# Kernel tuning notes

Measured on AMD Instinct MI355X. Metric: run time of the kernel, lower is better.

Reference implementation:

```python
import jax, jax.numpy as jnp
import numpy as np

EMBED = 768
HEADS = 32
HEAD_DIM = EMBED // HEADS  # 24
T = 512
B = 16


def setup_inputs() -> dict:
    key = jax.random.key(0)
    ks = jax.random.split(key, 10)
    s = 1.0 / np.sqrt(EMBED)
    inp = {
        "query": jax.random.normal(ks[0], (T, B, EMBED), dtype=jnp.float32),
        "attn_bias": jax.random.normal(ks[1], (B * HEADS, T, T), dtype=jnp.float32),
        "Wq": jax.random.normal(ks[2], (EMBED, EMBED), dtype=jnp.float32) * s,
        "bq": jnp.zeros((EMBED,), dtype=jnp.float32),
        "Wk": jax.random.normal(ks[3], (EMBED, EMBED), dtype=jnp.float32) * s,
        "bk": jnp.zeros((EMBED,), dtype=jnp.float32),
        "Wv": jax.random.normal(ks[4], (EMBED, EMBED), dtype=jnp.float32) * s,
        "bv": jnp.zeros((EMBED,), dtype=jnp.float32),
        "Wo": jax.random.normal(ks[5], (EMBED, EMBED), dtype=jnp.float32) * s,
        "bo": jnp.zeros((EMBED,), dtype=jnp.float32),
    }
    return inp


def _split_heads(x):
    # [T, B, E] -> [B, H, T, d]
    t, b, _ = x.shape
    return x.reshape(t, b, HEADS, HEAD_DIM).transpose(1, 2, 0, 3)


def reference(query, attn_bias, Wq, bq, Wk, bk, Wv, bv, Wo, bo):
    t, b, e = query.shape
    scaling = HEAD_DIM ** (-0.5)
    # projections (torch Linear: x @ W.T + b)
    q = (query @ Wq.T + bq) * scaling
    k = query @ Wk.T + bk
    v = query @ Wv.T + bv
    qh, kh, vh = _split_heads(q), _split_heads(k), _split_heads(v)  # [B,H,T,d]
    scores = jnp.einsum('bhtd,bhsd->bhts', qh, kh)
    scores = scores + attn_bias.reshape(b, HEADS, t, t)
    probs = jax.nn.softmax(scores, axis=-1)  # dropout = identity (eval)
    attn = jnp.einsum('bhts,bhsd->bhtd', probs, vh)  # [B,H,T,d]
    attn = attn.transpose(2, 0, 1, 3).reshape(t, b, e)  # [T,B,E]
    out = attn @ Wo.T + bo  # final dropout = identity (eval)
    return out
```

## Files before the change

### kernel.cpp

```cpp
#include <hip/hip_runtime.h>
#include <hip/hip_bf16.h>

#define T_SEQ 512
#define BATCH 16
#define EMB 768
#define HEADS 32
#define HDIM 24
#define ROWS (T_SEQ * BATCH)
#define SCALING 0.20412414523193154f

__global__ __launch_bounds__(256)
void qkv_proj_kernel(const float* __restrict__ X,
                     const float* __restrict__ Wq, const float* __restrict__ Wk,
                     const float* __restrict__ Wv,
                     const float* __restrict__ bq, const float* __restrict__ bk,
                     const float* __restrict__ bv,
                     float* __restrict__ qo, float* __restrict__ ko,
                     float* __restrict__ vo)
{
    __shared__ float Xs[64][17];
    __shared__ __attribute__((aligned(16))) float Ws[16][68];

    const int tid = threadIdx.x;
    const int r0 = blockIdx.x * 64;
    const int nb = blockIdx.y;
    const int which = nb / 12;
    const int n0 = (nb % 12) * 64;
    const float* W    = (which == 0) ? Wq : (which == 1) ? Wk : Wv;
    const float* bias = (which == 0) ? bq : (which == 1) ? bk : bv;
    float* out        = (which == 0) ? qo : (which == 1) ? ko : vo;

    const int lrow = tid >> 2;
    const int lcol = (tid & 3) << 2;
    const int tx = tid & 15;
    const int ty = tid >> 4;

    float acc[4][4] = {};

    for (int k0 = 0; k0 < EMB; k0 += 16) {
        const float4 xv = *(const float4*)(X + (size_t)(r0 + lrow) * EMB + k0 + lcol);
        const float4 wv = *(const float4*)(W + (size_t)(n0 + lrow) * EMB + k0 + lcol);
        Xs[lrow][lcol + 0] = xv.x; Xs[lrow][lcol + 1] = xv.y;
        Xs[lrow][lcol + 2] = xv.z; Xs[lrow][lcol + 3] = xv.w;
        Ws[lcol + 0][lrow] = wv.x; Ws[lcol + 1][lrow] = wv.y;
        Ws[lcol + 2][lrow] = wv.z; Ws[lcol + 3][lrow] = wv.w;
        __syncthreads();
#pragma unroll
        for (int kk = 0; kk < 16; ++kk) {
            const float4 b4 = *(const float4*)&Ws[kk][tx * 4];
            const float a0 = Xs[ty * 4 + 0][kk];
            const float a1 = Xs[ty * 4 + 1][kk];
            const float a2 = Xs[ty * 4 + 2][kk];
            const float a3 = Xs[ty * 4 + 3][kk];
            acc[0][0] += a0 * b4.x; acc[0][1] += a0 * b4.y; acc[0][2] += a0 * b4.z; acc[0][3] += a0 * b4.w;
            acc[1][0] += a1 * b4.x; acc[1][1] += a1 * b4.y; acc[1][2] += a1 * b4.z; acc[1][3] += a1 * b4.w;
            acc[2][0] += a2 * b4.x; acc[2][1] += a2 * b4.y; acc[2][2] += a2 * b4.z; acc[2][3] += a2 * b4.w;
            acc[3][0] += a3 * b4.x; acc[3][1] += a3 * b4.y; acc[3][2] += a3 * b4.z; acc[3][3] += a3 * b4.w;
        }
        __syncthreads();
    }

#pragma unroll
    for (int ii = 0; ii < 4; ++ii) {
        const int rr = r0 + ty * 4 + ii;
        const int t = rr >> 4;
        const int b = rr & 15;
#pragma unroll
        for (int jj = 0; jj < 4; ++jj) {
            const int nn = n0 + tx * 4 + jj;
            float c = acc[ii][jj] + bias[nn];
            if (which == 0) c *= SCALING;
            const int h = nn / HDIM;
            const int dd = nn - h * HDIM;
            out[((size_t)((b * HEADS + h) * T_SEQ + t)) * HDIM + dd] = c;
        }
    }
}

__global__ __launch_bounds__(256)
void attn_kernel(const float* __restrict__ qb, const float* __restrict__ kb,
                 const float* __restrict__ vb, const float* __restrict__ bias,
                 float* __restrict__ attn)
{
    const int bh = blockIdx.x;
    const int t0 = blockIdx.y * 16;
    const int tid = threadIdx.x;

    __shared__ float Qs[16][25];
    __shared__ float Ss[16][513];
    __shared__ float red[16][17];
    __shared__ float rowm[16];
    __shared__ float rowl[16];

    const float* Kb = kb + (size_t)bh * T_SEQ * HDIM;
    const float* Vb = vb + (size_t)bh * T_SEQ * HDIM;
    const float* Bb = bias + (size_t)bh * T_SEQ * T_SEQ + (size_t)t0 * T_SEQ;

    for (int e = tid; e < 16 * HDIM; e += 256) {
        const int i = e / HDIM, dd = e - i * HDIM;
        Qs[i][dd] = qb[((size_t)bh * T_SEQ + t0 + i) * HDIM + dd];
    }
    __syncthreads();

    for (int e = tid; e < 16 * T_SEQ; e += 256) {
        const int i = e >> 9, s = e & 511;
        const float* kr = Kb + s * HDIM;
        float d = 0.f;
#pragma unroll
        for (int dd = 0; dd < HDIM; ++dd) d += Qs[i][dd] * kr[dd];
        Ss[i][s] = d + Bb[i * T_SEQ + s];
    }
    __syncthreads();

    const int i = tid >> 4;
    const int g = tid & 15;
    float m = -1e30f;
    for (int s = g; s < T_SEQ; s += 16) m = fmaxf(m, Ss[i][s]);
    red[i][g] = m;
    __syncthreads();
    if (g == 0) {
        float mm = red[i][0];
#pragma unroll
        for (int j = 1; j < 16; ++j) mm = fmaxf(mm, red[i][j]);
        rowm[i] = mm;
    }
    __syncthreads();
    const float mrow = rowm[i];
    float l = 0.f;
    for (int s = g; s < T_SEQ; s += 16) {
        const float p = __expf(Ss[i][s] - mrow);
        Ss[i][s] = p;
        l += p;
    }
    red[i][g] = l;
    __syncthreads();
    if (g == 0) {
        float ll = 0.f;
#pragma unroll
        for (int j = 0; j < 16; ++j) ll += red[i][j];
        rowl[i] = 1.f / ll;
    }
    __syncthreads();

    for (int p = tid; p < 16 * HDIM; p += 256) {
        const int ii = p / HDIM, dd = p - ii * HDIM;
        float accv = 0.f;
        const float* vp = Vb + dd;
#pragma unroll 8
        for (int s = 0; s < T_SEQ; ++s) accv += Ss[ii][s] * vp[s * HDIM];
        accv *= rowl[ii];
        const int t = t0 + ii;
        const int b = bh >> 5;
        const int h = bh & 31;
        attn[((size_t)(t * BATCH + b)) * EMB + h * HDIM + dd] = accv;
    }
}

__global__ __launch_bounds__(256)
void out_proj_kernel(const float* __restrict__ A, const float* __restrict__ Wo,
                     const float* __restrict__ bo, float* __restrict__ out)
{
    __shared__ float Xs[64][17];
    __shared__ __attribute__((aligned(16))) float Ws[16][68];

    const int tid = threadIdx.x;
    const int r0 = blockIdx.x * 64;
    const int n0 = blockIdx.y * 64;

    const int lrow = tid >> 2;
    const int lcol = (tid & 3) << 2;
    const int tx = tid & 15;
    const int ty = tid >> 4;

    float acc[4][4] = {};

    for (int k0 = 0; k0 < EMB; k0 += 16) {
        const float4 xv = *(const float4*)(A + (size_t)(r0 + lrow) * EMB + k0 + lcol);
        const float4 wv = *(const float4*)(Wo + (size_t)(n0 + lrow) * EMB + k0 + lcol);
        Xs[lrow][lcol + 0] = xv.x; Xs[lrow][lcol + 1] = xv.y;
        Xs[lrow][lcol + 2] = xv.z; Xs[lrow][lcol + 3] = xv.w;
        Ws[lcol + 0][lrow] = wv.x; Ws[lcol + 1][lrow] = wv.y;
        Ws[lcol + 2][lrow] = wv.z; Ws[lcol + 3][lrow] = wv.w;
        __syncthreads();
#pragma unroll
        for (int kk = 0; kk < 16; ++kk) {
            const float4 b4 = *(const float4*)&Ws[kk][tx * 4];
            const float a0 = Xs[ty * 4 + 0][kk];
            const float a1 = Xs[ty * 4 + 1][kk];
            const float a2 = Xs[ty * 4 + 2][kk];
            const float a3 = Xs[ty * 4 + 3][kk];
            acc[0][0] += a0 * b4.x; acc[0][1] += a0 * b4.y; acc[0][2] += a0 * b4.z; acc[0][3] += a0 * b4.w;
            acc[1][0] += a1 * b4.x; acc[1][1] += a1 * b4.y; acc[1][2] += a1 * b4.z; acc[1][3] += a1 * b4.w;
            acc[2][0] += a2 * b4.x; acc[2][1] += a2 * b4.y; acc[2][2] += a2 * b4.z; acc[2][3] += a2 * b4.w;
            acc[3][0] += a3 * b4.x; acc[3][1] += a3 * b4.y; acc[3][2] += a3 * b4.z; acc[3][3] += a3 * b4.w;
        }
        __syncthreads();
    }

#pragma unroll
    for (int ii = 0; ii < 4; ++ii) {
        const int rr = r0 + ty * 4 + ii;
#pragma unroll
        for (int jj = 0; jj < 4; ++jj) {
            const int nn = n0 + tx * 4 + jj;
            out[(size_t)rr * EMB + nn] = acc[ii][jj] + bo[nn];
        }
    }
}

extern "C" void kernel_launch(void* const* d_in, const int* in_sizes, int n_in,
                              void* d_out, int out_size, void* d_ws, size_t ws_size,
                              hipStream_t stream)
{
    const float* query = (const float*)d_in[0];
    const float* abias = (const float*)d_in[1];
    const float* Wq = (const float*)d_in[2];
    const float* bq = (const float*)d_in[3];
    const float* Wk = (const float*)d_in[4];
    const float* bk = (const float*)d_in[5];
    const float* Wv = (const float*)d_in[6];
    const float* bv = (const float*)d_in[7];
    const float* Wo = (const float*)d_in[8];
    const float* bo = (const float*)d_in[9];
    float* out = (float*)d_out;

    float* ws = (float*)d_ws;
    const size_t QKV_ELEMS = (size_t)BATCH * HEADS * T_SEQ * HDIM;
    float* qb = ws;
    float* kb = ws + QKV_ELEMS;
    float* vb = ws + 2 * QKV_ELEMS;
    float* ab = ws + 3 * QKV_ELEMS;

    dim3 gA(ROWS / 64, 36);
    qkv_proj_kernel<<<gA, 256, 0, stream>>>(query, Wq, Wk, Wv, bq, bk, bv, qb, kb, vb);

    dim3 gB(BATCH * HEADS, T_SEQ / 16);
    attn_kernel<<<gB, 256, 0, stream>>>(qb, kb, vb, abias, ab);

    dim3 gC(ROWS / 64, EMB / 64);
    out_proj_kernel<<<gC, 256, 0, stream>>>(ab, Wo, bo, out);
}
```

Measured before the change: 2.357 ms.

## Stage K and V tiles in shared memory and restructure attention thread mapping

The attention kernel now loads K and V in 128-row tiles into shared memory with vectorized float4 loads, instead of having every thread read K and V rows straight from global memory. Each QK thread computes four scores per float4 bias load, and the block grows to 384 threads so each thread owns one (row, dim) output for PV. The grid is reordered so consecutive blocks share the same head, which should improve L2 reuse of K and V. The cost is extra shared memory and barriers, plus idle threads during the softmax phase.

```diff
diff --git a/kernel.cpp b/kernel.cpp
--- a/kernel.cpp
+++ b/kernel.cpp
@@ -77,17 +77,18 @@
     }
 }
 
-__global__ __launch_bounds__(256)
+__global__ __launch_bounds__(384)
 void attn_kernel(const float* __restrict__ qb, const float* __restrict__ kb,
                  const float* __restrict__ vb, const float* __restrict__ bias,
                  float* __restrict__ attn)
 {
-    const int bh = blockIdx.x;
-    const int t0 = blockIdx.y * 16;
+    const int t0 = blockIdx.x * 16;
+    const int bh = blockIdx.y;
     const int tid = threadIdx.x;
 
     __shared__ float Qs[16][25];
-    __shared__ float Ss[16][513];
+    __shared__ float Ss[16][521];
+    __shared__ __attribute__((aligned(16))) float Ts[128][28];
     __shared__ float red[16][17];
     __shared__ float rowm[16];
     __shared__ float rowl[16];
@@ -96,64 +97,101 @@
     const float* Vb = vb + (size_t)bh * T_SEQ * HDIM;
     const float* Bb = bias + (size_t)bh * T_SEQ * T_SEQ + (size_t)t0 * T_SEQ;
 
-    for (int e = tid; e < 16 * HDIM; e += 256) {
-        const int i = e / HDIM, dd = e - i * HDIM;
+    {
+        const int i = tid / HDIM, dd = tid - i * HDIM;
         Qs[i][dd] = qb[((size_t)bh * T_SEQ + t0 + i) * HDIM + dd];
     }
     __syncthreads();
 
-    for (int e = tid; e < 16 * T_SEQ; e += 256) {
-        const int i = e >> 9, s = e & 511;
-        const float* kr = Kb + s * HDIM;
-        float d = 0.f;
-#pragma unroll
-        for (int dd = 0; dd < HDIM; ++dd) d += Qs[i][dd] * kr[dd];
-        Ss[i][s] = d + Bb[i * T_SEQ + s];
-    }
-    __syncthreads();
-
-    const int i = tid >> 4;
-    const int g = tid & 15;
-    float m = -1e30f;
-    for (int s = g; s < T_SEQ; s += 16) m = fmaxf(m, Ss[i][s]);
-    red[i][g] = m;
-    __syncthreads();
-    if (g == 0) {
+    for (int tile = 0; tile < 4; ++tile) {
+        for (int fv = tid; fv < 768; fv += 384) {
+            const float4 kv = *(const float4*)(Kb + (size_t)tile * 3072 + (size_t)fv * 4);
+            const int row = fv / 6;
+            const int col = (fv - row * 6) * 4;
+            *(float4*)&Ts[row][col] = kv;
+        }
+        __syncthreads();
+        for (int f = tid; f < 512; f += 384) {
+            const int i = f >> 5;
+            const int sl = (f & 31) * 4;
+            const float4 bv = *(const float4*)(Bb + (size_t)i * T_SEQ + tile * 128 + sl);
+            float d0 = 0.f, d1 = 0.f, d2 = 0.f, d3 = 0.f;
+#pragma unroll
+            for (int dd = 0; dd < HDIM; ++dd) {
+                const float q = Qs[i][dd];
+                d0 += q * Ts[sl + 0][dd];
+                d1 += q * Ts[sl + 1][dd];
+                d2 += q * Ts[sl + 2][dd];
+                d3 += q * Ts[sl + 3][dd];
+            }
+            const int sg = tile * 128 + sl;
+            Ss[i][sg + 0] = d0 + bv.x;
+            Ss[i][sg + 1] = d1 + bv.y;
+            Ss[i][sg + 2] = d2 + bv.z;
+            Ss[i][sg + 3] = d3 + bv.w;
+        }
+        __syncthreads();
+    }
+
+    if (tid < 256) {
+        const int i = tid >> 4;
+        const int g = tid & 15;
+        float m = -1e30f;
+        for (int s = g; s < T_SEQ; s += 16) m = fmaxf(m, Ss[i][s]);
+        red[i][g] = m;
+    }
+    __syncthreads();
+    if (tid < 256 && (tid & 15) == 0) {
+        const int i = tid >> 4;
         float mm = red[i][0];
 #pragma unroll
         for (int j = 1; j < 16; ++j) mm = fmaxf(mm, red[i][j]);
         rowm[i] = mm;
     }
     __syncthreads();
-    const float mrow = rowm[i];
-    float l = 0.f;
-    for (int s = g; s < T_SEQ; s += 16) {
-        const float p = __expf(Ss[i][s] - mrow);
-        Ss[i][s] = p;
-        l += p;
-    }
-    red[i][g] = l;
-    __syncthreads();
-    if (g == 0) {
+    if (tid < 256) {
+        const int i = tid >> 4;
+        const int g = tid & 15;
+        const float mrow = rowm[i];
+        float l = 0.f;
+        for (int s = g; s < T_SEQ; s += 16) {
+            const float p = __expf(Ss[i][s] - mrow);
+            Ss[i][s] = p;
+            l += p;
+        }
+        red[i][g] = l;
+    }
+    __syncthreads();
+    if (tid < 256 && (tid & 15) == 0) {
+        const int i = tid >> 4;
         float ll = 0.f;
 #pragma unroll
         for (int j = 0; j < 16; ++j) ll += red[i][j];
         rowl[i] = 1.f / ll;
     }
-    __syncthreads();
-
-    for (int p = tid; p < 16 * HDIM; p += 256) {
-        const int ii = p / HDIM, dd = p - ii * HDIM;
-        float accv = 0.f;
-        const float* vp = Vb + dd;
-#pragma unroll 8
-        for (int s = 0; s < T_SEQ; ++s) accv += Ss[ii][s] * vp[s * HDIM];
-        accv *= rowl[ii];
-        const int t = t0 + ii;
-        const int b = bh >> 5;
-        const int h = bh & 31;
-        attn[((size_t)(t * BATCH + b)) * EMB + h * HDIM + dd] = accv;
-    }
+
+    const int pi = tid / HDIM;
+    const int pd = tid - pi * HDIM;
+    float accv = 0.f;
+    for (int tile = 0; tile < 4; ++tile) {
+        __syncthreads();
+        for (int fv = tid; fv < 768; fv += 384) {
+            const float4 vv = *(const float4*)(Vb + (size_t)tile * 3072 + (size_t)fv * 4);
+            const int row = fv / 6;
+            const int col = (fv - row * 6) * 4;
+            *(float4*)&Ts[row][col] = vv;
+        }
+        __syncthreads();
+        const int sbase = tile * 128;
+#pragma unroll 4
+        for (int sl = 0; sl < 128; ++sl) {
+            accv += Ss[pi][sbase + sl] * Ts[sl][pd];
+        }
+    }
+    accv *= rowl[pi];
+    const int b = bh >> 5;
+    const int h = bh & 31;
+    attn[((size_t)((t0 + pi) * BATCH + b)) * EMB + h * HDIM + pd] = accv;
 }
 
 __global__ __launch_bounds__(256)
@@ -234,8 +272,8 @@
     dim3 gA(ROWS / 64, 36);
     qkv_proj_kernel<<<gA, 256, 0, stream>>>(query, Wq, Wk, Wv, bq, bk, bv, qb, kb, vb);
 
-    dim3 gB(BATCH * HEADS, T_SEQ / 16);
-    attn_kernel<<<gB, 256, 0, stream>>>(qb, kb, vb, abias, ab);
+    dim3 gB(T_SEQ / 16, BATCH * HEADS);
+    attn_kernel<<<gB, 384, 0, stream>>>(qb, kb, vb, abias, ab);
 
     dim3 gC(ROWS / 64, EMB / 64);
     out_proj_kernel<<<gC, 256, 0, stream>>>(ab, Wo, bo, out);
```

Result: slower. 3.023 ms (+28.2%).
